# Performance work log

Measured on AMD Instinct MI355X. Metric: run time of the kernel, lower is better.

Reference implementation:

```python
import jax, jax.numpy as jnp
import numpy as np

EPS = 1e-12  # torch F.normalize default eps

def _l1_normalize(x):
    # F.normalize(x, p=1, dim=1): divide by channel-wise L1 norm, clamped at eps
    n = jnp.sum(jnp.abs(x), axis=1, keepdims=True)
    return x / jnp.maximum(n, EPS)

def setup_inputs() -> dict:
    key = jax.random.key(0)
    k1, k2, k3 = jax.random.split(key, 3)
    shape = (2, 128, 64, 64)  # B, C, H, W
    return {
        "a": jax.random.normal(k1, shape, dtype=jnp.float32),
        "b": jax.random.normal(k2, shape, dtype=jnp.float32),
        "c": jax.random.normal(k3, shape, dtype=jnp.float32),
    }

def reference(a, b, c):
    a = _l1_normalize(a)
    b = _l1_normalize(b)
    c = _l1_normalize(c)
    sim_ab = jnp.einsum('bchw,bcij->bhwij', a, b)
    sim_ac = jnp.einsum('bchw,bcij->bhwij', a, c)
    # F.l1_loss default reduction='mean'
    return jnp.mean(jnp.abs(sim_ac - sim_ab))
```

## Files before the change

### kernel.cpp

```cpp
#include <hip/hip_runtime.h>
#include <stdint.h>

#define HW 4096
#define NC 128
#define BATCH 2

typedef __attribute__((ext_vector_type(8))) short bf16x8;
typedef __attribute__((ext_vector_type(4))) float f32x4;
typedef __attribute__((ext_vector_type(8))) unsigned short u16x8;

__device__ __forceinline__ unsigned short f32_to_bf16(float f) {
    union { float f; unsigned int u; } v; v.f = f;
    unsigned int u = v.u;
    unsigned int r = (u + 0x7FFFu + ((u >> 16) & 1u)) >> 16;
    return (unsigned short)r;
}

__global__ __launch_bounds__(256) void norm_kernel(
    const float* __restrict__ A, const float* __restrict__ B,
    const float* __restrict__ Cc,
    unsigned short* __restrict__ anT, unsigned short* __restrict__ dT,
    float* __restrict__ out) {
    const int tid = threadIdx.x;
    if (blockIdx.x == 0 && tid == 0) *out = 0.f;
    const int pl = tid & 31;
    const int cp = tid >> 5;
    const int gp = blockIdx.x * 32;
    const int bb = gp >> 12;
    const int p  = (gp & (HW - 1)) + pl;
    const size_t base = (size_t)bb * NC * HW + p;
    const int c0 = cp * 16;

    float va[16], vb[16], vc[16];
    float sa = 0.f, sb = 0.f, sc = 0.f;
#pragma unroll
    for (int k = 0; k < 16; ++k) {
        size_t idx = base + (size_t)(c0 + k) * HW;
        va[k] = A[idx]; vb[k] = B[idx]; vc[k] = Cc[idx];
        sa += fabsf(va[k]); sb += fabsf(vb[k]); sc += fabsf(vc[k]);
    }
    __shared__ float red[3][8][32];
    red[0][cp][pl] = sa; red[1][cp][pl] = sb; red[2][cp][pl] = sc;
    __syncthreads();
    float na = 0.f, nb = 0.f, nc = 0.f;
#pragma unroll
    for (int g = 0; g < 8; ++g) {
        na += red[0][g][pl]; nb += red[1][g][pl]; nc += red[2][g][pl];
    }
    const float ra = 1.f / fmaxf(na, 1e-12f);
    const float rb = 1.f / fmaxf(nb, 1e-12f);
    const float rc = 1.f / fmaxf(nc, 1e-12f);

    const size_t obase = ((size_t)bb * HW + p) * NC;
    const int sw = p & 15;
#pragma unroll
    for (int c8 = 0; c8 < 2; ++c8) {
        u16x8 xa, xd;
#pragma unroll
        for (int j = 0; j < 8; ++j) {
            int k = c8 * 8 + j;
            xa[j] = f32_to_bf16(va[k] * ra);
            xd[j] = f32_to_bf16(vc[k] * rc - vb[k] * rb);
        }
        const int slot = (cp * 2 + c8) ^ sw;
        *(u16x8*)(anT + obase + slot * 8) = xa;
        *(u16x8*)(dT  + obase + slot * 8) = xd;
    }
}

__global__ __launch_bounds__(256, 2) void simloss_kernel(
    const unsigned short* __restrict__ anT, const unsigned short* __restrict__ dT,
    float* __restrict__ out) {
    __shared__ uint4 smem4[4096];
    const int tid = threadIdx.x;
    const int bz  = blockIdx.z;
    const int m0  = blockIdx.y * 128;
    const int n0  = blockIdx.x * 128;
    const uint4* gA = (const uint4*)(anT + ((size_t)bz * HW + m0) * NC);
    const uint4* gB = (const uint4*)(dT  + ((size_t)bz * HW + n0) * NC);
#pragma unroll
    for (int i = 0; i < 8; ++i) {
        int idx = i * 256 + tid;
        smem4[idx]        = gA[idx];
        smem4[2048 + idx] = gB[idx];
    }
    __syncthreads();

    const int ln   = tid & 63;
    const int wv   = tid >> 6;
    const int m16  = ln & 15;
    const int quad = ln >> 4;
    const int wr   = (wv >> 1) * 64;
    const int wc   = (wv & 1) * 64;
    const uint8_t* As = (const uint8_t*)smem4;
    const uint8_t* Bs = (const uint8_t*)(smem4 + 2048);

    f32x4 acc[4][4] = {};
#pragma unroll
    for (int ks = 0; ks < 4; ++ks) {
        const int chunk = ks * 4 + quad;
        const int slot  = chunk ^ m16;
        bf16x8 af[4], bfr[4];
#pragma unroll
        for (int mi = 0; mi < 4; ++mi)
            af[mi] = *(const bf16x8*)(As + (wr + mi * 16 + m16) * 256 + slot * 16);
#pragma unroll
        for (int ni = 0; ni < 4; ++ni)
            bfr[ni] = *(const bf16x8*)(Bs + (wc + ni * 16 + m16) * 256 + slot * 16);
#pragma unroll
        for (int mi = 0; mi < 4; ++mi)
#pragma unroll
            for (int ni = 0; ni < 4; ++ni)
                acc[mi][ni] = __builtin_amdgcn_mfma_f32_16x16x32_bf16(
                    af[mi], bfr[ni], acc[mi][ni], 0, 0, 0);
    }

    float s = 0.f;
#pragma unroll
    for (int mi = 0; mi < 4; ++mi)
#pragma unroll
        for (int ni = 0; ni < 4; ++ni)
#pragma unroll
            for (int r = 0; r < 4; ++r)
                s += fabsf(acc[mi][ni][r]);
#pragma unroll
    for (int off = 32; off > 0; off >>= 1)
        s += __shfl_down(s, off);

    __syncthreads();
    if (ln == 0) ((float*)smem4)[wv] = s;
    __syncthreads();
    if (tid == 0) {
        const float inv = 1.0f / ((float)BATCH * (float)HW * (float)HW);
        float t = ((float*)smem4)[0] + ((float*)smem4)[1] +
                  ((float*)smem4)[2] + ((float*)smem4)[3];
        atomicAdd(out, t * inv);
    }
}

extern "C" void kernel_launch(void* const* d_in, const int* in_sizes, int n_in,
                              void* d_out, int out_size, void* d_ws, size_t ws_size,
                              hipStream_t stream) {
    const float* A  = (const float*)d_in[0];
    const float* B  = (const float*)d_in[1];
    const float* Cc = (const float*)d_in[2];
    float* out = (float*)d_out;
    unsigned short* anT = (unsigned short*)d_ws;
    unsigned short* dT  = anT + (size_t)BATCH * HW * NC;

    norm_kernel<<<dim3(256), dim3(256), 0, stream>>>(A, B, Cc, anT, dT, out);
    simloss_kernel<<<dim3(32, 32, BATCH), dim3(256), 0, stream>>>(anT, dT, out);
}
```

Measured before the change: 95.18 us.

## Reuse A tile across four B tiles with async global-to-LDS loads

Each simloss block now keeps one 128-row A tile in LDS and walks four consecutive B tiles, so the grid shrinks from 2048 blocks to 512 and each A tile is loaded once per four output tiles. Tile loads go through the global_load_lds builtin, which writes straight into LDS without staging through registers. The norm kernel moves to 512 threads, each handling 8 channels and writing one 16-byte vector per output. In exchange the B reloads are not double-buffered, so loads and MFMA work run back to back with barriers between them, and there are fewer blocks to hide latency.

```diff
diff --git a/kernel.cpp b/kernel.cpp
--- a/kernel.cpp
+++ b/kernel.cpp
@@ -16,7 +16,13 @@
     return (unsigned short)r;
 }
 
-__global__ __launch_bounds__(256) void norm_kernel(
+__device__ __forceinline__ void async_cp16(const void* g, void* s) {
+    __builtin_amdgcn_global_load_lds(
+        (const __attribute__((address_space(1))) uint32_t*)g,
+        (__attribute__((address_space(3))) uint32_t*)s, 16, 0, 0);
+}
+
+__global__ __launch_bounds__(512) void norm_kernel(
     const float* __restrict__ A, const float* __restrict__ B,
     const float* __restrict__ Cc,
     unsigned short* __restrict__ anT, unsigned short* __restrict__ dT,
@@ -24,27 +30,27 @@
     const int tid = threadIdx.x;
     if (blockIdx.x == 0 && tid == 0) *out = 0.f;
     const int pl = tid & 31;
-    const int cp = tid >> 5;
+    const int cg = tid >> 5;
     const int gp = blockIdx.x * 32;
     const int bb = gp >> 12;
     const int p  = (gp & (HW - 1)) + pl;
     const size_t base = (size_t)bb * NC * HW + p;
-    const int c0 = cp * 16;
+    const int c0 = cg * 8;
 
-    float va[16], vb[16], vc[16];
+    float va[8], vb[8], vc[8];
     float sa = 0.f, sb = 0.f, sc = 0.f;
 #pragma unroll
-    for (int k = 0; k < 16; ++k) {
+    for (int k = 0; k < 8; ++k) {
         size_t idx = base + (size_t)(c0 + k) * HW;
         va[k] = A[idx]; vb[k] = B[idx]; vc[k] = Cc[idx];
         sa += fabsf(va[k]); sb += fabsf(vb[k]); sc += fabsf(vc[k]);
     }
-    __shared__ float red[3][8][32];
-    red[0][cp][pl] = sa; red[1][cp][pl] = sb; red[2][cp][pl] = sc;
+    __shared__ float red[3][16][32];
+    red[0][cg][pl] = sa; red[1][cg][pl] = sb; red[2][cg][pl] = sc;
     __syncthreads();
     float na = 0.f, nb = 0.f, nc = 0.f;
 #pragma unroll
-    for (int g = 0; g < 8; ++g) {
+    for (int g = 0; g < 16; ++g) {
         na += red[0][g][pl]; nb += red[1][g][pl]; nc += red[2][g][pl];
     }
     const float ra = 1.f / fmaxf(na, 1e-12f);
@@ -52,20 +58,15 @@
     const float rc = 1.f / fmaxf(nc, 1e-12f);
 
     const size_t obase = ((size_t)bb * HW + p) * NC;
-    const int sw = p & 15;
+    const int slot = cg ^ (p & 15);
+    u16x8 xa, xd;
 #pragma unroll
-    for (int c8 = 0; c8 < 2; ++c8) {
-        u16x8 xa, xd;
-#pragma unroll
-        for (int j = 0; j < 8; ++j) {
-            int k = c8 * 8 + j;
-            xa[j] = f32_to_bf16(va[k] * ra);
-            xd[j] = f32_to_bf16(vc[k] * rc - vb[k] * rb);
-        }
-        const int slot = (cp * 2 + c8) ^ sw;
-        *(u16x8*)(anT + obase + slot * 8) = xa;
-        *(u16x8*)(dT  + obase + slot * 8) = xd;
+    for (int j = 0; j < 8; ++j) {
+        xa[j] = f32_to_bf16(va[j] * ra);
+        xd[j] = f32_to_bf16(vc[j] * rc - vb[j] * rb);
     }
+    *(u16x8*)(anT + obase + slot * 8) = xa;
+    *(u16x8*)(dT  + obase + slot * 8) = xd;
 }
 
 __global__ __launch_bounds__(256, 2) void simloss_kernel(
@@ -73,61 +74,77 @@
     float* __restrict__ out) {
     __shared__ uint4 smem4[4096];
     const int tid = threadIdx.x;
-    const int bz  = blockIdx.z;
-    const int m0  = blockIdx.y * 128;
-    const int n0  = blockIdx.x * 128;
-    const uint4* gA = (const uint4*)(anT + ((size_t)bz * HW + m0) * NC);
-    const uint4* gB = (const uint4*)(dT  + ((size_t)bz * HW + n0) * NC);
+    const int b   = blockIdx.x;
+    const int bz  = b >> 8;
+    const int my  = (b & 255) >> 3;
+    const int ng  = b & 7;
+    const char* gA = (const char*)(anT + ((size_t)bz * HW + my * 128) * NC);
+    const char* gB0 = (const char*)(dT + ((size_t)bz * HW + ng * 4 * 128) * NC);
+
+    const int wv  = tid >> 6;
+    const int ln  = tid & 63;
+    char* sA = (char*)smem4;
+    char* sB = (char*)(smem4 + 2048);
+
 #pragma unroll
     for (int i = 0; i < 8; ++i) {
-        int idx = i * 256 + tid;
-        smem4[idx]        = gA[idx];
-        smem4[2048 + idx] = gB[idx];
+        const size_t goff = (size_t)(i * 256 + tid) * 16;
+        const size_t loff = (size_t)i * 4096 + wv * 1024;
+        async_cp16(gA + goff, sA + loff);
+        async_cp16(gB0 + goff, sB + loff);
     }
     __syncthreads();
 
-    const int ln   = tid & 63;
-    const int wv   = tid >> 6;
     const int m16  = ln & 15;
     const int quad = ln >> 4;
     const int wr   = (wv >> 1) * 64;
     const int wc   = (wv & 1) * 64;
-    const uint8_t* As = (const uint8_t*)smem4;
-    const uint8_t* Bs = (const uint8_t*)(smem4 + 2048);
 
-    f32x4 acc[4][4] = {};
+    float s = 0.f;
+    for (int j = 0; j < 4; ++j) {
+        f32x4 acc[4][4] = {};
 #pragma unroll
-    for (int ks = 0; ks < 4; ++ks) {
-        const int chunk = ks * 4 + quad;
-        const int slot  = chunk ^ m16;
-        bf16x8 af[4], bfr[4];
+        for (int ks = 0; ks < 4; ++ks) {
+            const int chunk = ks * 4 + quad;
+            const int slot  = chunk ^ m16;
+            bf16x8 af[4], bfr[4];
 #pragma unroll
-        for (int mi = 0; mi < 4; ++mi)
-            af[mi] = *(const bf16x8*)(As + (wr + mi * 16 + m16) * 256 + slot * 16);
+            for (int mi = 0; mi < 4; ++mi)
+                af[mi] = *(const bf16x8*)(sA + (wr + mi * 16 + m16) * 256 + slot * 16);
 #pragma unroll
-        for (int ni = 0; ni < 4; ++ni)
-            bfr[ni] = *(const bf16x8*)(Bs + (wc + ni * 16 + m16) * 256 + slot * 16);
+            for (int ni = 0; ni < 4; ++ni)
+                bfr[ni] = *(const bf16x8*)(sB + (wc + ni * 16 + m16) * 256 + slot * 16);
+#pragma unroll
+            for (int mi = 0; mi < 4; ++mi)
+#pragma unroll
+                for (int ni = 0; ni < 4; ++ni)
+                    acc[mi][ni] = __builtin_amdgcn_mfma_f32_16x16x32_bf16(
+                        af[mi], bfr[ni], acc[mi][ni], 0, 0, 0);
+        }
 #pragma unroll
         for (int mi = 0; mi < 4; ++mi)
 #pragma unroll
             for (int ni = 0; ni < 4; ++ni)
-                acc[mi][ni] = __builtin_amdgcn_mfma_f32_16x16x32_bf16(
-                    af[mi], bfr[ni], acc[mi][ni], 0, 0, 0);
+#pragma unroll
+                for (int r = 0; r < 4; ++r)
+                    s += fabsf(acc[mi][ni][r]);
+
+        __syncthreads();
+        if (j < 3) {
+            const char* gBn = gB0 + (size_t)(j + 1) * 32768;
+#pragma unroll
+            for (int i = 0; i < 8; ++i) {
+                const size_t goff = (size_t)(i * 256 + tid) * 16;
+                const size_t loff = (size_t)i * 4096 + wv * 1024;
+                async_cp16(gBn + goff, sB + loff);
+            }
+            __syncthreads();
+        }
     }
 
-    float s = 0.f;
-#pragma unroll
-    for (int mi = 0; mi < 4; ++mi)
-#pragma unroll
-        for (int ni = 0; ni < 4; ++ni)
-#pragma unroll
-            for (int r = 0; r < 4; ++r)
-                s += fabsf(acc[mi][ni][r]);
 #pragma unroll
     for (int off = 32; off > 0; off >>= 1)
         s += __shfl_down(s, off);
-
-    __syncthreads();
     if (ln == 0) ((float*)smem4)[wv] = s;
     __syncthreads();
     if (tid == 0) {
@@ -148,6 +165,6 @@
     unsigned short* anT = (unsigned short*)d_ws;
     unsigned short* dT  = anT + (size_t)BATCH * HW * NC;
 
-    norm_kernel<<<dim3(256), dim3(256), 0, stream>>>(A, B, Cc, anT, dT, out);
-    simloss_kernel<<<dim3(32, 32, BATCH), dim3(256), 0, stream>>>(anT, dT, out);
+    norm_kernel<<<dim3(256), dim3(512), 0, stream>>>(A, B, Cc, anT, dT, out);
+    simloss_kernel<<<dim3(512), dim3(256), 0, stream>>>(anT, dT, out);
 }
```

New measurement: 79.90 us. 1.19x faster.
